# Optimization experiments

Hardware: AMD Instinct MI355X
Metric: run time of the kernel (lower is better)

Reference implementation:

```python
import jax, jax.numpy as jnp
import numpy as np

N = 50000
NEG_SLOPE_ATT = 0.2   # GATv2 attention leaky_relu slope (PyG default)
NEG_SLOPE_ACT = 0.01  # F.leaky_relu default between layers


def setup_inputs() -> dict:
    key = jax.random.key(0)
    ks = jax.random.split(key, 16)
    d = 128
    E = 800000
    s = 0.1  # weight scale for numerical sanity
    inp = {
        "x": jax.random.normal(ks[0], (N, d), jnp.float32),
        "edge_index": jax.random.randint(ks[1], (2, E), 0, N, jnp.int64),
        "Wl0": jax.random.normal(ks[2], (d, d), jnp.float32) * s,
        "bl0": jnp.zeros((d,), jnp.float32),
        "Wr0": jax.random.normal(ks[3], (d, d), jnp.float32) * s,
        "br0": jnp.zeros((d,), jnp.float32),
        "att0": jax.random.normal(ks[4], (d,), jnp.float32) * s,
        "bo0": jnp.zeros((d,), jnp.float32),
        "Wl1": jax.random.normal(ks[5], (d, d), jnp.float32) * s,
        "bl1": jnp.zeros((d,), jnp.float32),
        "Wr1": jax.random.normal(ks[6], (d, d), jnp.float32) * s,
        "br1": jnp.zeros((d,), jnp.float32),
        "att1": jax.random.normal(ks[7], (d,), jnp.float32) * s,
        "bo1": jnp.zeros((d,), jnp.float32),
    }
    return inp


def gatv2_conv(x, Wl, bl, Wr, br, att, bo, src, dst):
    # GATv2Conv, heads=1, add_self_loops handled by caller (src/dst already include them).
    xl = x @ Wl + bl            # [N, H] source-side transform (message payload)
    xr = x @ Wr + br            # [N, H] target-side transform
    m = jax.nn.leaky_relu(xl[src] + xr[dst], NEG_SLOPE_ATT)  # [E, H]
    e = m @ att                 # [E] attention logits
    # segment softmax over incoming edges of each destination node
    emax = jax.ops.segment_max(e, dst, num_segments=N)
    ex = jnp.exp(e - emax[dst])
    denom = jax.ops.segment_sum(ex, dst, num_segments=N)
    alpha = ex / (denom[dst] + 1e-16)
    out = jax.ops.segment_sum(xl[src] * alpha[:, None], dst, num_segments=N)
    return out + bo


def reference(x, edge_index, Wl0, bl0, Wr0, br0, att0, bo0,
              Wl1, bl1, Wr1, br1, att1, bo1):
    # add self-loops once (GATv2Conv default add_self_loops=True)
    loop = jnp.arange(N, dtype=edge_index.dtype)
    src = jnp.concatenate([edge_index[0], loop])
    dst = jnp.concatenate([edge_index[1], loop])

    h = gatv2_conv(x, Wl0, bl0, Wr0, br0, att0, bo0, src, dst)
    h = jax.nn.leaky_relu(h, NEG_SLOPE_ACT)
    # F.dropout(training=False) -> identity
    out = gatv2_conv(h, Wl1, bl1, Wr1, br1, att1, bo1, src, dst)
    return out
```

## Files before the change

### kernel.cpp

```cpp
#include <hip/hip_runtime.h>
#include <hip/hip_bf16.h>
#include <math.h>


#define LRELU_ATT 0.2f
#define LRELU_ACT 0.01f

typedef __attribute__((ext_vector_type(8))) short bf16x8;
typedef __attribute__((ext_vector_type(4))) float f32x4;
typedef __attribute__((ext_vector_type(2))) float f32x2;

#define SORT_BLOCKS 256
#define BUCKET_CAP  8192


__device__ __forceinline__ unsigned short f2bf(float f) {
    unsigned u = __float_as_uint(f);
    unsigned r = (u + 0x7fffu + ((u >> 16) & 1u)) >> 16;
    return (unsigned short)r;
}

__device__ __forceinline__ bf16x8 pack8(float4 a, float4 b) {
    union { bf16x8 v; unsigned short u[8]; } t;
    t.u[0] = f2bf(a.x); t.u[1] = f2bf(a.y); t.u[2] = f2bf(a.z); t.u[3] = f2bf(a.w);
    t.u[4] = f2bf(b.x); t.u[5] = f2bf(b.y); t.u[6] = f2bf(b.z); t.u[7] = f2bf(b.w);
    return t.v;
}

__device__ __forceinline__ bf16x8 ldbf8(const unsigned short* p) {
    union { uint4 q; bf16x8 v; } t;
    t.q = *(const uint4*)p;
    return t.v;
}

__device__ __forceinline__ void unpack8p(uint4 q, f32x2* v) {
    f32x2 a;
    a.x = __uint_as_float(q.x << 16); a.y = __uint_as_float(q.x & 0xffff0000u); v[0] = a;
    a.x = __uint_as_float(q.y << 16); a.y = __uint_as_float(q.y & 0xffff0000u); v[1] = a;
    a.x = __uint_as_float(q.z << 16); a.y = __uint_as_float(q.z & 0xffff0000u); v[2] = a;
    a.x = __uint_as_float(q.w << 16); a.y = __uint_as_float(q.w & 0xffff0000u); v[3] = a;
}

__device__ __forceinline__ float logit8p(const f32x2* v, const f32x2* xr2,
                                         const f32x2* at2) {
    f32x2 p; p.x = 0.f; p.y = 0.f;
    #pragma unroll
    for (int j = 0; j < 4; ++j) {
        f32x2 m = v[j] + xr2[j];
        f32x2 mm = __builtin_elementwise_max(m, m * LRELU_ATT);
        p = mm * at2[j] + p;
    }
    return p.x + p.y;
}


__global__ __launch_bounds__(256) void histA_wconv_kernel(
    const int* __restrict__ ei, int E, int Etot, int chunk, int nbuck,
    int* __restrict__ histmat,
    const float* __restrict__ W0, const float* __restrict__ W1,
    const float* __restrict__ W2, const float* __restrict__ W3,
    unsigned short* __restrict__ Wb) {
    __shared__ int h[256];
    const int tid = threadIdx.x;
    if (blockIdx.x < SORT_BLOCKS) {
        h[tid] = 0;
        __syncthreads();
        const int b0 = blockIdx.x * chunk;
        const int b1 = min(b0 + chunk, Etot);
        for (int e = b0 + tid; e < b1; e += 256) {
            int d = (e < E) ? ei[E + e] : (e - E);
            atomicAdd(&h[d >> 8], 1);
        }
        __syncthreads();
        if (tid < nbuck) histmat[tid * SORT_BLOCKS + blockIdx.x] = h[tid];
    } else {
        int g = (blockIdx.x - SORT_BLOCKS) * 256 + tid;
        int m = g >> 14;
        int f = g & 16383;
        int j = f & 7, l = (f >> 3) & 63, ct = (f >> 9) & 7, ks = f >> 12;
        int row = ks * 32 + ((l >> 4) << 3) + j;
        int col = ct * 16 + (l & 15);
        const float* W = m == 0 ? W0 : m == 1 ? W1 : m == 2 ? W2 : W3;
        Wb[g] = f2bf(W[row * 128 + col]);
    }
}

__global__ __launch_bounds__(256) void scanB1_kernel(
    const int* __restrict__ histmat, int* __restrict__ btot) {
    __shared__ int s[256];
    const int b = blockIdx.x, tid = threadIdx.x;
    s[tid] = histmat[b * SORT_BLOCKS + tid];
    __syncthreads();
    #pragma unroll
    for (int d = 128; d > 0; d >>= 1) {
        if (tid < d) s[tid] += s[tid + d];
        __syncthreads();
    }
    if (tid == 0) btot[b] = s[0];
}

__global__ __launch_bounds__(256) void scanB3_kernel(
    int* __restrict__ histmat, const int* __restrict__ btot, int nbuck,
    int* __restrict__ bbase) {
    __shared__ int s[256];
    const int b = blockIdx.x, tid = threadIdx.x;

    int v = (tid < nbuck) ? btot[tid] : 0;
    s[tid] = v;
    __syncthreads();
    int sum = v;
    #pragma unroll
    for (int d = 1; d < 256; d <<= 1) {
        int t = (tid >= d) ? s[tid - d] : 0;
        __syncthreads();
        sum += t;
        s[tid] = sum;
        __syncthreads();
    }
    const int base = (b > 0) ? s[b - 1] : 0;
    if (tid == 0) {
        bbase[b] = base;
        if (b == nbuck - 1) bbase[nbuck] = s[nbuck - 1];
    }
    __syncthreads();

    const int rv = histmat[b * SORT_BLOCKS + tid];
    s[tid] = rv;
    __syncthreads();
    int rsum = rv;
    #pragma unroll
    for (int d = 1; d < 256; d <<= 1) {
        int t = (tid >= d) ? s[tid - d] : 0;
        __syncthreads();
        rsum += t;
        s[tid] = rsum;
        __syncthreads();
    }
    histmat[b * SORT_BLOCKS + tid] = base + rsum - rv;
}


template<bool INF32>
__device__ __forceinline__ void gemm_body(
    int gblk, const void* __restrict__ Xin,
    const unsigned short* __restrict__ Wb,
    const float* __restrict__ bl, const float* __restrict__ br,
    unsigned short* __restrict__ xlb, unsigned short* __restrict__ xrb, int n) {
    const int tid  = threadIdx.x;
    const int wave = tid >> 6, lane = tid & 63;
    const int rowbase = gblk * 128 + wave * 32;
    const int lrow = lane & 15;
    const int kgrp = lane >> 4;

    bf16x8 af[2][4];
    #pragma unroll
    for (int rt = 0; rt < 2; ++rt) {
        const int row = rowbase + rt * 16 + lrow;
        const bool ok = row < n;
        #pragma unroll
        for (int ks = 0; ks < 4; ++ks) {
            const int k0 = ks * 32 + kgrp * 8;
            if (INF32) {
                const float* X = (const float*)Xin;
                float4 a = make_float4(0.f, 0.f, 0.f, 0.f), b = a;
                if (ok) {
                    a = *(const float4*)(X + (size_t)row * 128 + k0);
                    b = *(const float4*)(X + (size_t)row * 128 + k0 + 4);
                }
                af[rt][ks] = pack8(a, b);
            } else {
                const unsigned short* X = (const unsigned short*)Xin;
                union { uint4 q; bf16x8 v; } t;
                t.q = make_uint4(0u, 0u, 0u, 0u);
                if (ok) t.q = *(const uint4*)(X + (size_t)row * 128 + k0);
                af[rt][ks] = t.v;
            }
        }
    }

    #pragma unroll
    for (int m = 0; m < 2; ++m) {
        const unsigned short* wb = Wb + m * 16384;
        f32x4 acc[2][8];
        #pragma unroll
        for (int rt = 0; rt < 2; ++rt)
            #pragma unroll
            for (int ct = 0; ct < 8; ++ct)
                acc[rt][ct] = (f32x4){0.f, 0.f, 0.f, 0.f};

        #pragma unroll
        for (int ct = 0; ct < 8; ++ct) {
            #pragma unroll
            for (int ks = 0; ks < 4; ++ks) {
                bf16x8 bf = ldbf8(wb + ((ks * 8 + ct) * 64 + lane) * 8);
                acc[0][ct] = __builtin_amdgcn_mfma_f32_16x16x32_bf16(af[0][ks], bf, acc[0][ct], 0, 0, 0);
                acc[1][ct] = __builtin_amdgcn_mfma_f32_16x16x32_bf16(af[1][ks], bf, acc[1][ct], 0, 0, 0);
            }
        }

        const float* bias = m ? br : bl;
        unsigned short* dst = m ? xrb : xlb;
        #pragma unroll
        for (int rt = 0; rt < 2; ++rt) {
            #pragma unroll
            for (int ct = 0; ct < 8; ++ct) {
                const int col = ct * 16 + lrow;
                const float bv = bias[col];
                #pragma unroll
                for (int i = 0; i < 4; ++i) {
                    const int row = rowbase + rt * 16 + kgrp * 4 + i;
                    if (row < n)
                        dst[(size_t)row * 128 + col] = f2bf(acc[rt][ct][i] + bv);
                }
            }
        }
    }
}

template<bool INF32>
__global__ __launch_bounds__(256) void gemm_mfma_kernel(
    const void* __restrict__ Xin, const unsigned short* __restrict__ Wb,
    const float* __restrict__ bl, const float* __restrict__ br,
    unsigned short* __restrict__ xlb, unsigned short* __restrict__ xrb, int n) {
    gemm_body<INF32>(blockIdx.x, Xin, Wb, bl, br, xlb, xrb, n);
}

__global__ __launch_bounds__(256) void scatter_gemm_kernel(
    const int* __restrict__ ei, int E, int Etot, int chunk, int nbuck,
    const int* __restrict__ histmat, unsigned* __restrict__ ebuf,
    const float* __restrict__ X, const unsigned short* __restrict__ Wb,
    const float* __restrict__ bl, const float* __restrict__ br,
    unsigned short* __restrict__ xlb, unsigned short* __restrict__ xrb, int n) {
    if (blockIdx.x < SORT_BLOCKS) {
        __shared__ int cur[256];
        const int tid = threadIdx.x;
        if (tid < nbuck) cur[tid] = histmat[tid * SORT_BLOCKS + blockIdx.x];
        __syncthreads();
        const int b0 = blockIdx.x * chunk;
        const int b1 = min(b0 + chunk, Etot);
        for (int e = b0 + tid; e < b1; e += 256) {
            int s, d;
            if (e < E) { s = ei[e]; d = ei[E + e]; }
            else       { s = d = e - E; }
            int pos = atomicAdd(&cur[d >> 8], 1);
            ebuf[pos] = ((unsigned)(d & 255) << 16) | (unsigned)s;
        }
    } else {
        gemm_body<true>(blockIdx.x - SORT_BLOCKS, (const void*)X, Wb, bl, br,
                        xlb, xrb, n);
    }
}

__global__ __launch_bounds__(512) void bucket_csr_kernel(
    const unsigned* __restrict__ ebuf, const int* __restrict__ bbase, int n,
    int nbuck, int* __restrict__ offs, int* __restrict__ colsrc) {
    __shared__ int cnt[256];
    __shared__ int cur[256];
    __shared__ unsigned eb[BUCKET_CAP];
    const int b = blockIdx.x, tid = threadIdx.x;
    const int lo = bbase[b], hi = bbase[b + 1];
    const int m = hi - lo;
    const int node0 = b << 8;
    const bool inl = (m <= BUCKET_CAP);

    if (tid < 256) cnt[tid] = 0;
    __syncthreads();

    if (inl) {
        for (int i = tid; i < m; i += 512) {
            unsigned q = ebuf[lo + i];
            eb[i] = q;
            atomicAdd(&cnt[q >> 16], 1);
        }
    } else {
        for (int i = tid; i < m; i += 512)
            atomicAdd(&cnt[ebuf[lo + i] >> 16], 1);
    }
    __syncthreads();

    const int deg = (tid < 256) ? cnt[tid] : 0;
    if (tid < 256) cur[tid] = deg;
    __syncthreads();
    int sum = deg;
    #pragma unroll
    for (int d = 1; d < 256; d <<= 1) {
        int t = 0;
        if (tid < 256 && tid >= d) t = cur[tid - d];
        __syncthreads();
        if (tid < 256) { sum += t; cur[tid] = sum; }
        __syncthreads();
    }
    if (tid < 256) {
        int off = lo + sum - deg;
        if (node0 + tid < n) offs[node0 + tid] = off;
        cur[tid] = off;
    }
    if (b == nbuck - 1 && tid == 0) offs[n] = hi;
    __syncthreads();

    if (inl) {
        for (int i = tid; i < m; i += 512) {
            unsigned q = eb[i];
            int pos = atomicAdd(&cur[q >> 16], 1);
            colsrc[pos] = (int)(q & 0xffffu);
        }
    } else {
        for (int i = tid; i < m; i += 512) {
            unsigned q = ebuf[lo + i];
            int pos = atomicAdd(&cur[q >> 16], 1);
            colsrc[pos] = (int)(q & 0xffffu);
        }
    }
}


template<bool OUTBF>
__global__ __launch_bounds__(256) void gat_agg_kernel(
    const unsigned short* __restrict__ xlb, const unsigned short* __restrict__ xrb,
    const float* __restrict__ att, const float* __restrict__ bo,
    const int* __restrict__ offs, const int* __restrict__ col,
    float* __restrict__ outf, unsigned short* __restrict__ outb,
    int n, int apply_act) {
    const int lane = threadIdx.x & 63;
    const int sub  = lane >> 4;
    const int sl   = lane & 15;
    const int gw   = (blockIdx.x * blockDim.x + threadIdx.x) >> 6;
    const int node = gw * 4 + sub;
    const bool valid = node < n;

    const uint4* xq = (const uint4*)xlb;
    const float4* att4 = (const float4*)att;
    f32x2 xr2[4], at2[4];
    {
        uint4 qa = make_uint4(0u, 0u, 0u, 0u);
        if (valid) qa = ((const uint4*)xrb)[(size_t)node * 16 + sl];
        unpack8p(qa, xr2);
        float4 c = att4[sl * 2], d = att4[sl * 2 + 1];
        at2[0].x = c.x; at2[0].y = c.y; at2[1].x = c.z; at2[1].y = c.w;
        at2[2].x = d.x; at2[2].y = d.y; at2[3].x = d.z; at2[3].y = d.w;
    }

    f32x2 acc[4];
    #pragma unroll
    for (int j = 0; j < 4; ++j) { acc[j].x = 0.f; acc[j].y = 0.f; }
    float den = 0.f;

    int b = 0, cnt = 0;
    if (valid) { b = offs[node]; cnt = offs[node + 1] - b; }

    int t = 0;
    for (; t + 2 <= cnt; t += 2) {
        const int s0 = col[b + t], s1 = col[b + t + 1];
        uint4 q0 = xq[(size_t)s0 * 16 + sl];
        uint4 q1 = xq[(size_t)s1 * 16 + sl];
        f32x2 v0[4], v1[4];
        unpack8p(q0, v0);
        unpack8p(q1, v1);
        float p0 = logit8p(v0, xr2, at2);
        float p1 = logit8p(v1, xr2, at2);
        p0 += __shfl_xor(p0, 1, 64);  p1 += __shfl_xor(p1, 1, 64);
        p0 += __shfl_xor(p0, 2, 64);  p1 += __shfl_xor(p1, 2, 64);
        p0 += __shfl_xor(p0, 4, 64);  p1 += __shfl_xor(p1, 4, 64);
        p0 += __shfl_xor(p0, 8, 64);  p1 += __shfl_xor(p1, 8, 64);
        const float e0 = __expf(p0), e1 = __expf(p1);
        #pragma unroll
        for (int j = 0; j < 4; ++j) {
            acc[j] = v0[j] * e0 + acc[j];
            acc[j] = v1[j] * e1 + acc[j];
        }
        den += e0 + e1;
    }
    if (t < cnt) {
        const int s0 = col[b + t];
        uint4 q0 = xq[(size_t)s0 * 16 + sl];
        f32x2 v0[4];
        unpack8p(q0, v0);
        float p0 = logit8p(v0, xr2, at2);
        p0 += __shfl_xor(p0, 1, 64);
        p0 += __shfl_xor(p0, 2, 64);
        p0 += __shfl_xor(p0, 4, 64);
        p0 += __shfl_xor(p0, 8, 64);
        const float e0 = __expf(p0);
        #pragma unroll
        for (int j = 0; j < 4; ++j) acc[j] = v0[j] * e0 + acc[j];
        den += e0;
    }

    if (valid) {
        const float inv = 1.f / (den + 1e-16f);
        float4 b1 = ((const float4*)bo)[sl * 2];
        float4 b2 = ((const float4*)bo)[sl * 2 + 1];
        float bov[8] = {b1.x, b1.y, b1.z, b1.w, b2.x, b2.y, b2.z, b2.w};
        float o[8];
        #pragma unroll
        for (int j = 0; j < 4; ++j) {
            o[2 * j]     = acc[j].x * inv + bov[2 * j];
            o[2 * j + 1] = acc[j].y * inv + bov[2 * j + 1];
        }
        if (apply_act) {
            #pragma unroll
            for (int j = 0; j < 8; ++j) o[j] = o[j] > 0.f ? o[j] : LRELU_ACT * o[j];
        }
        if (OUTBF) {
            ushort4 u0, u1;
            u0.x = f2bf(o[0]); u0.y = f2bf(o[1]); u0.z = f2bf(o[2]); u0.w = f2bf(o[3]);
            u1.x = f2bf(o[4]); u1.y = f2bf(o[5]); u1.z = f2bf(o[6]); u1.w = f2bf(o[7]);
            ushort4* ob = (ushort4*)(outb + (size_t)node * 128 + sl * 8);
            ob[0] = u0; ob[1] = u1;
        } else {
            float4* o4 = (float4*)(outf + (size_t)node * 128 + sl * 8);
            o4[0] = make_float4(o[0], o[1], o[2], o[3]);
            o4[1] = make_float4(o[4], o[5], o[6], o[7]);
        }
    }
}


static inline size_t align_up(size_t x, size_t a) { return (x + a - 1) & ~(a - 1); }

extern "C" void kernel_launch(void* const* d_in, const int* in_sizes, int n_in,
                              void* d_out, int out_size, void* d_ws, size_t ws_size,
                              hipStream_t stream) {
    const float* x   = (const float*)d_in[0];
    const int*   ei  = (const int*)d_in[1];
    const float* Wl0 = (const float*)d_in[2];
    const float* bl0 = (const float*)d_in[3];
    const float* Wr0 = (const float*)d_in[4];
    const float* br0 = (const float*)d_in[5];
    const float* att0= (const float*)d_in[6];
    const float* bo0 = (const float*)d_in[7];
    const float* Wl1 = (const float*)d_in[8];
    const float* bl1 = (const float*)d_in[9];
    const float* Wr1 = (const float*)d_in[10];
    const float* br1 = (const float*)d_in[11];
    const float* att1= (const float*)d_in[12];
    const float* bo1 = (const float*)d_in[13];
    float* outp = (float*)d_out;

    const int N     = in_sizes[0] / 128;
    const int E     = in_sizes[1] / 2;
    const int Etot  = E + N;
    const int NBUCK = (N + 255) >> 8;
    const int CHUNK = (Etot + SORT_BLOCKS - 1) / SORT_BLOCKS;

    char* p = (char*)d_ws;
    size_t off = 0;
    unsigned short* xlb = (unsigned short*)(p + off);
    off = align_up(off + (size_t)N * 128 * 2, 256);
    unsigned short* xrb = (unsigned short*)(p + off);
    off = align_up(off + (size_t)N * 128 * 2, 256);
    unsigned short* Wb = (unsigned short*)(p + off);
    off = align_up(off + (size_t)4 * 16384 * 2, 256);
    int* histmat= (int*)(p + off); off = align_up(off + (size_t)NBUCK * SORT_BLOCKS * 4, 256);
    int* btot   = (int*)(p + off); off = align_up(off + (size_t)NBUCK * 4, 256);
    int* bbase  = (int*)(p + off); off = align_up(off + (size_t)(NBUCK + 1) * 4, 256);
    int* offs   = (int*)(p + off); off = align_up(off + (size_t)(N + 1) * 4, 256);
    int* colsrc = (int*)(p + off); off = align_up(off + (size_t)Etot * 4, 256);
    unsigned* ebuf = (unsigned*)(p + off); off = align_up(off + (size_t)Etot * 4, 256);
    unsigned short* hb = (unsigned short*)d_out;
    (void)ws_size;

    const int nbGemm = (N + 127) / 128;

    histA_wconv_kernel<<<SORT_BLOCKS + 256, 256, 0, stream>>>(
        ei, E, Etot, CHUNK, NBUCK, histmat, Wl0, Wr0, Wl1, Wr1, Wb);
    scanB1_kernel<<<NBUCK, 256, 0, stream>>>(histmat, btot);
    scanB3_kernel<<<NBUCK, 256, 0, stream>>>(histmat, btot, NBUCK, bbase);
    scatter_gemm_kernel<<<SORT_BLOCKS + nbGemm, 256, 0, stream>>>(
        ei, E, Etot, CHUNK, NBUCK, histmat, ebuf,
        x, Wb, bl0, br0, xlb, xrb, N);
    bucket_csr_kernel<<<NBUCK, 512, 0, stream>>>(ebuf, bbase, N, NBUCK, offs, colsrc);

    const int nbAgg = (N + 15) / 16;

    gat_agg_kernel<true><<<nbAgg, 256, 0, stream>>>(
        xlb, xrb, att0, bo0, offs, colsrc, nullptr, hb, N, 1);

    gemm_mfma_kernel<false><<<nbGemm, 256, 0, stream>>>(
        (const void*)hb, Wb + 2 * 16384, bl1, br1, xlb, xrb, N);
    gat_agg_kernel<false><<<nbAgg, 256, 0, stream>>>(
        xlb, xrb, att1, bo1, offs, colsrc, outp, nullptr, N, 0);
}
```

Before: 165.2 us.

## Merge scan kernels and split each node's edges across two half-waves

Folds the two-pass bucket scan into one kernel. Each block recomputes all bucket totals by reading the histogram rows with vector loads, and the per-block positions go to a separate buffer so the kernel does not overwrite data other blocks still read. The aggregation kernel now gives each node 32 lanes instead of 16 and processes four edges per iteration across two 16-lane subgroups, combining partial sums with cross-lane shuffles. This removes one launch and aims to raise memory parallelism per node, at the cost of twice as many aggregation blocks, redundant scan reads, and wasted lanes on low-degree nodes.

After: 162.2 us, median of 3. Within noise of the previous version (-1.9%).

```diff
diff --git a/kernel.cpp b/kernel.cpp
--- a/kernel.cpp
+++ b/kernel.cpp
@@ -85,30 +85,24 @@
     }
 }
 
-__global__ __launch_bounds__(256) void scanB1_kernel(
-    const int* __restrict__ histmat, int* __restrict__ btot) {
+__global__ __launch_bounds__(256) void scanB_kernel(
+    const int* __restrict__ histmat, int nbuck,
+    int* __restrict__ histpos, int* __restrict__ bbase) {
     __shared__ int s[256];
     const int b = blockIdx.x, tid = threadIdx.x;
-    s[tid] = histmat[b * SORT_BLOCKS + tid];
-    __syncthreads();
-    #pragma unroll
-    for (int d = 128; d > 0; d >>= 1) {
-        if (tid < d) s[tid] += s[tid + d];
-        __syncthreads();
-    }
-    if (tid == 0) btot[b] = s[0];
-}
-
-__global__ __launch_bounds__(256) void scanB3_kernel(
-    int* __restrict__ histmat, const int* __restrict__ btot, int nbuck,
-    int* __restrict__ bbase) {
-    __shared__ int s[256];
-    const int b = blockIdx.x, tid = threadIdx.x;
-
-    int v = (tid < nbuck) ? btot[tid] : 0;
-    s[tid] = v;
-    __syncthreads();
-    int sum = v;
+
+    int total = 0;
+    if (tid < nbuck) {
+        const int4* p = (const int4*)(histmat + tid * SORT_BLOCKS);
+        #pragma unroll 8
+        for (int k = 0; k < SORT_BLOCKS / 4; ++k) {
+            int4 v = p[k];
+            total += v.x + v.y + v.z + v.w;
+        }
+    }
+    s[tid] = total;
+    __syncthreads();
+    int sum = total;
     #pragma unroll
     for (int d = 1; d < 256; d <<= 1) {
         int t = (tid >= d) ? s[tid - d] : 0;
@@ -136,7 +130,7 @@
         s[tid] = rsum;
         __syncthreads();
     }
-    histmat[b * SORT_BLOCKS + tid] = base + rsum - rv;
+    histpos[b * SORT_BLOCKS + tid] = base + rsum - rv;
 }
 
 
@@ -227,14 +221,14 @@
 
 __global__ __launch_bounds__(256) void scatter_gemm_kernel(
     const int* __restrict__ ei, int E, int Etot, int chunk, int nbuck,
-    const int* __restrict__ histmat, unsigned* __restrict__ ebuf,
+    const int* __restrict__ histpos, unsigned* __restrict__ ebuf,
     const float* __restrict__ X, const unsigned short* __restrict__ Wb,
     const float* __restrict__ bl, const float* __restrict__ br,
     unsigned short* __restrict__ xlb, unsigned short* __restrict__ xrb, int n) {
     if (blockIdx.x < SORT_BLOCKS) {
         __shared__ int cur[256];
         const int tid = threadIdx.x;
-        if (tid < nbuck) cur[tid] = histmat[tid * SORT_BLOCKS + blockIdx.x];
+        if (tid < nbuck) cur[tid] = histpos[tid * SORT_BLOCKS + blockIdx.x];
         __syncthreads();
         const int b0 = blockIdx.x * chunk;
         const int b1 = min(b0 + chunk, Etot);
@@ -322,10 +316,11 @@
     float* __restrict__ outf, unsigned short* __restrict__ outb,
     int n, int apply_act) {
     const int lane = threadIdx.x & 63;
-    const int sub  = lane >> 4;
+    const int nh   = lane >> 5;
+    const int ss   = (lane >> 4) & 1;
     const int sl   = lane & 15;
     const int gw   = (blockIdx.x * blockDim.x + threadIdx.x) >> 6;
-    const int node = gw * 4 + sub;
+    const int node = gw * 2 + nh;
     const bool valid = node < n;
 
     const uint4* xq = (const uint4*)xlb;
@@ -348,9 +343,12 @@
     int b = 0, cnt = 0;
     if (valid) { b = offs[node]; cnt = offs[node + 1] - b; }
 
-    int t = 0;
-    for (; t + 2 <= cnt; t += 2) {
-        const int s0 = col[b + t], s1 = col[b + t + 1];
+    for (int k = 0; k < cnt; k += 4) {
+        const int k0 = k + ss;
+        const int k1 = k + 2 + ss;
+        const bool e0v = k0 < cnt, e1v = k1 < cnt;
+        const int s0 = col[b + (e0v ? k0 : 0)];
+        const int s1 = col[b + (e1v ? k1 : 0)];
         uint4 q0 = xq[(size_t)s0 * 16 + sl];
         uint4 q1 = xq[(size_t)s1 * 16 + sl];
         f32x2 v0[4], v1[4];
@@ -362,7 +360,8 @@
         p0 += __shfl_xor(p0, 2, 64);  p1 += __shfl_xor(p1, 2, 64);
         p0 += __shfl_xor(p0, 4, 64);  p1 += __shfl_xor(p1, 4, 64);
         p0 += __shfl_xor(p0, 8, 64);  p1 += __shfl_xor(p1, 8, 64);
-        const float e0 = __expf(p0), e1 = __expf(p1);
+        const float e0 = e0v ? __expf(p0) : 0.f;
+        const float e1 = e1v ? __expf(p1) : 0.f;
         #pragma unroll
         for (int j = 0; j < 4; ++j) {
             acc[j] = v0[j] * e0 + acc[j];
@@ -370,23 +369,15 @@
         }
         den += e0 + e1;
     }
-    if (t < cnt) {
-        const int s0 = col[b + t];
-        uint4 q0 = xq[(size_t)s0 * 16 + sl];
-        f32x2 v0[4];
-        unpack8p(q0, v0);
-        float p0 = logit8p(v0, xr2, at2);
-        p0 += __shfl_xor(p0, 1, 64);
-        p0 += __shfl_xor(p0, 2, 64);
-        p0 += __shfl_xor(p0, 4, 64);
-        p0 += __shfl_xor(p0, 8, 64);
-        const float e0 = __expf(p0);
-        #pragma unroll
-        for (int j = 0; j < 4; ++j) acc[j] = v0[j] * e0 + acc[j];
-        den += e0;
-    }
-
-    if (valid) {
+
+    den += __shfl_xor(den, 16, 64);
+    #pragma unroll
+    for (int j = 0; j < 4; ++j) {
+        acc[j].x += __shfl_xor(acc[j].x, 16, 64);
+        acc[j].y += __shfl_xor(acc[j].y, 16, 64);
+    }
+
+    if (valid && ss == 0) {
         const float inv = 1.f / (den + 1e-16f);
         float4 b1 = ((const float4*)bo)[sl * 2];
         float4 b2 = ((const float4*)bo)[sl * 2 + 1];
@@ -452,7 +443,7 @@
     unsigned short* Wb = (unsigned short*)(p + off);
     off = align_up(off + (size_t)4 * 16384 * 2, 256);
     int* histmat= (int*)(p + off); off = align_up(off + (size_t)NBUCK * SORT_BLOCKS * 4, 256);
-    int* btot   = (int*)(p + off); off = align_up(off + (size_t)NBUCK * 4, 256);
+    int* histpos= (int*)(p + off); off = align_up(off + (size_t)NBUCK * SORT_BLOCKS * 4, 256);
     int* bbase  = (int*)(p + off); off = align_up(off + (size_t)(NBUCK + 1) * 4, 256);
     int* offs   = (int*)(p + off); off = align_up(off + (size_t)(N + 1) * 4, 256);
     int* colsrc = (int*)(p + off); off = align_up(off + (size_t)Etot * 4, 256);
@@ -464,14 +455,13 @@
 
     histA_wconv_kernel<<<SORT_BLOCKS + 256, 256, 0, stream>>>(
         ei, E, Etot, CHUNK, NBUCK, histmat, Wl0, Wr0, Wl1, Wr1, Wb);
-    scanB1_kernel<<<NBUCK, 256, 0, stream>>>(histmat, btot);
-    scanB3_kernel<<<NBUCK, 256, 0, stream>>>(histmat, btot, NBUCK, bbase);
+    scanB_kernel<<<NBUCK, 256, 0, stream>>>(histmat, NBUCK, histpos, bbase);
     scatter_gemm_kernel<<<SORT_BLOCKS + nbGemm, 256, 0, stream>>>(
-        ei, E, Etot, CHUNK, NBUCK, histmat, ebuf,
+        ei, E, Etot, CHUNK, NBUCK, histpos, ebuf,
         x, Wb, bl0, br0, xlb, xrb, N);
     bucket_csr_kernel<<<NBUCK, 512, 0, stream>>>(ebuf, bbase, N, NBUCK, offs, colsrc);
 
-    const int nbAgg = (N + 15) / 16;
+    const int nbAgg = (N + 7) / 8;
 
     gat_agg_kernel<true><<<nbAgg, 256, 0, stream>>>(
         xlb, xrb, att0, bo0, offs, colsrc, nullptr, hb, N, 1);
```
